# Optimization experiments

Hardware: AMD Instinct MI355X
Metric: run time of the kernel (lower is better)

## Reference

```python
import jax, jax.numpy as jnp
import numpy as np

C = 64          # num_activations
SIZE = 51       # spline coefficients per activation
RANGE = 1.0
GRID = 2.0 * RANGE / (SIZE - 1)
EVEN = (SIZE % 2 == 0)


def setup_inputs() -> dict:
    key = jax.random.key(0)
    k1, k2 = jax.random.split(key)
    x = jax.random.normal(k1, (32, C, 128, 128), dtype=jnp.float32)
    # parameter: raw B-spline coefficients (flattened [C*SIZE]), relu-init style perturbed
    grid_tensor = jnp.broadcast_to(jnp.linspace(-RANGE, RANGE, SIZE, dtype=jnp.float32), (C, SIZE))
    coefficients_vect = (jax.nn.relu(grid_tensor) + 0.01 * jax.random.normal(k2, (C, SIZE), dtype=jnp.float32)).reshape(-1)
    scaling_coeffs_vect = jnp.ones((1, C, 1, 1), dtype=jnp.float32)
    return {"x": x, "coefficients_vect": coefficients_vect, "scaling_coeffs_vect": scaling_coeffs_vect}


def _lipschitz_vect(coefficients_vect):
    # slope_clipping: clamp consecutive slopes to [0, GRID], rebuild by cumsum, center at middle knot
    cs = coefficients_vect.reshape(C, SIZE)
    new_slopes = jnp.clip(cs[:, 1:] - cs[:, :-1], 0.0, GRID)
    new_cs = jnp.concatenate([jnp.zeros((C, 1), cs.dtype), jnp.cumsum(new_slopes, axis=1)], axis=1)
    new_cs = new_cs - new_cs[:, SIZE // 2][:, None]
    return new_cs.reshape(-1)


def reference(x, coefficients_vect, scaling_coeffs_vect):
    cv = _lipschitz_vect(coefficients_vect)
    zero_knot_indexes = jnp.arange(C, dtype=jnp.int32) * SIZE + SIZE // 2  # [C]
    xs = x * scaling_coeffs_vect
    max_range = GRID * (SIZE // 2 - 1)
    xq = xs
    if EVEN:
        xq = xq - GRID / 2
        max_range = GRID * (SIZE // 2 - 2)
    x_clamped = jnp.clip(xq, -(GRID * (SIZE // 2)), max_range)
    floored = jnp.floor(x_clamped / GRID)
    fracs = xq / GRID - floored  # NOTE: uses unclamped x, as in the torch code
    idx = (zero_knot_indexes[None, :, None, None] + floored).astype(jnp.int32)  # [N,C,H,W]
    out = cv[idx + 1] * fracs + cv[idx] * (1.0 - fracs)
    if EVEN:
        out = out + GRID / 2
    return out / scaling_coeffs_vect
```

## Files before the change

kernel.cpp:

```cpp
#include <hip/hip_runtime.h>

#define C_NUM 64
#define S_SIZE 51

#define GRID_F   0.04f
#define Q_LO    -25.0f
#define Q_HI     24.0f

__global__ __launch_bounds__(256) void linearspline_fwd(
    const float* __restrict__ x,
    const float* __restrict__ coef,
    const float* __restrict__ scale,
    float* __restrict__ out,
    int nvec)
{
    __shared__ float s_cs[C_NUM * S_SIZE];
    __shared__ float s_cv[C_NUM * S_SIZE];
    __shared__ float s_s[C_NUM];
    __shared__ float s_inv[C_NUM];

    for (int i = threadIdx.x; i < C_NUM * S_SIZE; i += 256) s_cs[i] = coef[i];
    if (threadIdx.x < C_NUM) {
        float s = scale[threadIdx.x];
        s_s[threadIdx.x]   = s;
        s_inv[threadIdx.x] = 1.0f / s;
    }
    __syncthreads();

    if (threadIdx.x < C_NUM) {
        const float* p = &s_cs[threadIdx.x * S_SIZE];
        float*       q = &s_cv[threadIdx.x * S_SIZE];
        float acc = 0.0f;
        q[0] = 0.0f;
        for (int j = 0; j < S_SIZE - 1; ++j) {
            float sl = p[j + 1] - p[j];
            sl = fminf(fmaxf(sl, 0.0f), GRID_F);
            acc += sl;
            q[j + 1] = acc;
        }
        float ctr = q[S_SIZE / 2];
        for (int j = 0; j < S_SIZE; ++j) q[j] -= ctr;
    }
    __syncthreads();

    const float4* xv = (const float4*)x;
    float4*       ov = (float4*)out;
    const int stride = gridDim.x * blockDim.x;

    for (int i = blockIdx.x * blockDim.x + threadIdx.x; i < nvec; i += stride) {
        const int c      = (i >> 12) & (C_NUM - 1);
        const float s    = s_s[c];
        const float inv  = s_inv[c];
        const float* cvc = &s_cv[c * S_SIZE];

        float4 v = xv[i];
        float4 r;
        float* vp = (float*)&v;
        float* rp = (float*)&r;
#pragma unroll
        for (int k = 0; k < 4; ++k) {
            float xs = vp[k] * s;
            float d  = xs / GRID_F;
            float dc = fminf(fmaxf(d, Q_LO), Q_HI);
            float fl = floorf(dc);
            float fr = d - fl;
            int   il = 25 + (int)fl;
            float a  = cvc[il];
            float b  = cvc[il + 1];
            rp[k] = (b * fr + a * (1.0f - fr)) * inv;
        }
        ov[i] = r;
    }
}

extern "C" void kernel_launch(void* const* d_in, const int* in_sizes, int n_in,
                              void* d_out, int out_size, void* d_ws, size_t ws_size,
                              hipStream_t stream) {
    const float* x     = (const float*)d_in[0];
    const float* coef  = (const float*)d_in[1];
    const float* scale = (const float*)d_in[2];
    float*       out   = (float*)d_out;

    const int n    = in_sizes[0];
    const int nvec = n >> 2;

    int blocks = (nvec + 255) / 256;
    if (blocks > 2048) blocks = 2048;

    linearspline_fwd<<<blocks, 256, 0, stream>>>(x, coef, scale, out, nvec);
}
```

Before: 242.3 us.

## Precompute projected spline coefficients in a separate kernel and streamline the main loop

Moves the slope clipping, cumulative sum and scale reciprocal into a one-block pre-kernel that writes its results to workspace. The main kernel then only copies the finished table into shared memory, so the 2048 blocks no longer each repeat a serial 51-step cumsum. The main loop also replaces the divide by the grid step with a multiply by 25, handles two float4s per iteration, writes output with nontemporal stores, and computes the channel once per thread. Computing the channel once relies on the grid stride being a multiple of the channel period, which only holds for this launch shape. The change adds an extra kernel launch and a global round trip for the table.

```diff
diff --git a/kernel.cpp b/kernel.cpp
--- a/kernel.cpp
+++ b/kernel.cpp
@@ -1,30 +1,24 @@
 #include <hip/hip_runtime.h>
 
-#define C_NUM 64
+#define C_NUM  64
 #define S_SIZE 51
 
-#define GRID_F   0.04f
-#define Q_LO    -25.0f
-#define Q_HI     24.0f
+#define GRID_F     0.04f
+#define INV_GRID_F 25.0f
+#define Q_LO      -25.0f
+#define Q_HI       24.0f
 
-__global__ __launch_bounds__(256) void linearspline_fwd(
-    const float* __restrict__ x,
+typedef float nfloat4 __attribute__((ext_vector_type(4)));
+
+__global__ __launch_bounds__(256) void spline_project(
     const float* __restrict__ coef,
     const float* __restrict__ scale,
-    float* __restrict__ out,
-    int nvec)
+    float* __restrict__ ws)
 {
     __shared__ float s_cs[C_NUM * S_SIZE];
     __shared__ float s_cv[C_NUM * S_SIZE];
-    __shared__ float s_s[C_NUM];
-    __shared__ float s_inv[C_NUM];
 
     for (int i = threadIdx.x; i < C_NUM * S_SIZE; i += 256) s_cs[i] = coef[i];
-    if (threadIdx.x < C_NUM) {
-        float s = scale[threadIdx.x];
-        s_s[threadIdx.x]   = s;
-        s_inv[threadIdx.x] = 1.0f / s;
-    }
     __syncthreads();
 
     if (threadIdx.x < C_NUM) {
@@ -40,36 +34,73 @@
         }
         float ctr = q[S_SIZE / 2];
         for (int j = 0; j < S_SIZE; ++j) q[j] -= ctr;
+
+        float s = scale[threadIdx.x];
+        ws[C_NUM * S_SIZE + threadIdx.x]          = s;
+        ws[C_NUM * S_SIZE + C_NUM + threadIdx.x]  = 1.0f / s;
     }
     __syncthreads();
 
-    const float4* xv = (const float4*)x;
-    float4*       ov = (float4*)out;
+    for (int i = threadIdx.x; i < C_NUM * S_SIZE; i += 256) ws[i] = s_cv[i];
+}
+
+__device__ __forceinline__ nfloat4 spline4(nfloat4 v, float s, float inv, const float* __restrict__ cvc)
+{
+    nfloat4 r;
+#pragma unroll
+    for (int k = 0; k < 4; ++k) {
+        float xs = v[k] * s;
+        float d  = xs * INV_GRID_F;
+        float dc = fminf(fmaxf(d, Q_LO), Q_HI);
+        float fl = floorf(dc);
+        float fr = d - fl;
+        int   il = 25 + (int)fl;
+        float a  = cvc[il];
+        float b  = cvc[il + 1];
+        r[k] = (b * fr + a * (1.0f - fr)) * inv;
+    }
+    return r;
+}
+
+__global__ __launch_bounds__(256, 8) void linearspline_fwd(
+    const float* __restrict__ x,
+    const float* __restrict__ ws,
+    float* __restrict__ out,
+    int nvec)
+{
+    __shared__ float s_cv[C_NUM * S_SIZE];
+    __shared__ float s_s[C_NUM];
+    __shared__ float s_inv[C_NUM];
+
+    for (int i = threadIdx.x; i < C_NUM * S_SIZE; i += 256) s_cv[i] = ws[i];
+    if (threadIdx.x < C_NUM) {
+        s_s[threadIdx.x]   = ws[C_NUM * S_SIZE + threadIdx.x];
+        s_inv[threadIdx.x] = ws[C_NUM * S_SIZE + C_NUM + threadIdx.x];
+    }
+    __syncthreads();
+
+    const nfloat4* xv = (const nfloat4*)x;
+    nfloat4*       ov = (nfloat4*)out;
     const int stride = gridDim.x * blockDim.x;
+    int i = blockIdx.x * blockDim.x + threadIdx.x;
 
-    for (int i = blockIdx.x * blockDim.x + threadIdx.x; i < nvec; i += stride) {
-        const int c      = (i >> 12) & (C_NUM - 1);
-        const float s    = s_s[c];
-        const float inv  = s_inv[c];
-        const float* cvc = &s_cv[c * S_SIZE];
+    const int   c   = (i >> 12) & (C_NUM - 1);
+    const float s   = s_s[c];
+    const float inv = s_inv[c];
+    const float* cvc = &s_cv[c * S_SIZE];
 
-        float4 v = xv[i];
-        float4 r;
-        float* vp = (float*)&v;
-        float* rp = (float*)&r;
-#pragma unroll
-        for (int k = 0; k < 4; ++k) {
-            float xs = vp[k] * s;
-            float d  = xs / GRID_F;
-            float dc = fminf(fmaxf(d, Q_LO), Q_HI);
-            float fl = floorf(dc);
-            float fr = d - fl;
-            int   il = 25 + (int)fl;
-            float a  = cvc[il];
-            float b  = cvc[il + 1];
-            rp[k] = (b * fr + a * (1.0f - fr)) * inv;
-        }
-        ov[i] = r;
+    for (; i + stride < nvec; i += 2 * stride) {
+        nfloat4 v0 = xv[i];
+        nfloat4 v1 = xv[i + stride];
+        nfloat4 r0 = spline4(v0, s, inv, cvc);
+        nfloat4 r1 = spline4(v1, s, inv, cvc);
+        __builtin_nontemporal_store(r0, &ov[i]);
+        __builtin_nontemporal_store(r1, &ov[i + stride]);
+    }
+    for (; i < nvec; i += stride) {
+        nfloat4 v = xv[i];
+        nfloat4 r = spline4(v, s, inv, cvc);
+        __builtin_nontemporal_store(r, &ov[i]);
     }
 }
 
@@ -80,12 +111,12 @@
     const float* coef  = (const float*)d_in[1];
     const float* scale = (const float*)d_in[2];
     float*       out   = (float*)d_out;
+    float*       ws    = (float*)d_ws;
 
     const int n    = in_sizes[0];
     const int nvec = n >> 2;
 
-    int blocks = (nvec + 255) / 256;
-    if (blocks > 2048) blocks = 2048;
+    spline_project<<<1, 256, 0, stream>>>(coef, scale, ws);
 
-    linearspline_fwd<<<blocks, 256, 0, stream>>>(x, coef, scale, out, nvec);
+    linearspline_fwd<<<2048, 256, 0, stream>>>(x, ws, out, nvec);
 }
```

New measurement: 247.6 us. +2.2%, slower.
